# Kernel optimization log

Hardware: AMD Instinct MI355X
Metric: run time of the kernel (lower is better)

The kernel has to match this reference:

```python
import jax, jax.numpy as jnp
import numpy as np

N = 100000   # nodes
E = 800000   # directed edges
IN = 256     # in_channels (== hidden, required by repo's vn MLP dims)
HID = 256    # hidden_channels
OUT = 40     # out_channels (arxiv classes)
EPS = 1e-5


def setup_inputs() -> dict:
    key = jax.random.key(0)
    ks = jax.random.split(key, 8)
    def nrm(k, shape, scale=0.05):
        return jax.random.normal(k, shape, dtype=jnp.float32) * scale
    return {
        "x": nrm(ks[0], (N, IN), 1.0),
        "edge_index": jax.random.randint(ks[1], (2, E), 0, N, dtype=jnp.int32),
        # GCNConv weights (PyG: x @ W, then normalized aggregation, then + bias)
        "W0": nrm(ks[2], (IN, HID)),  "b0": jnp.zeros((HID,), jnp.float32),
        "W1": nrm(ks[3], (HID, HID)), "b1": jnp.zeros((HID,), jnp.float32),
        "W2": nrm(ks[4], (HID, OUT)), "b2": jnp.zeros((OUT,), jnp.float32),
        # BatchNorm1d affine params (batch-stat math, training mode)
        "bn_g0": jnp.ones((HID,), jnp.float32), "bn_b0": jnp.zeros((HID,), jnp.float32),
        "bn_g1": jnp.ones((HID,), jnp.float32), "bn_b1": jnp.zeros((HID,), jnp.float32),
        # virtual node embedding (init to 0 per reset_parameters)
        "vn_emb": jnp.zeros((1, IN), jnp.float32),
        # mlp_vns[0]: Linear(IN,HID) + LayerNorm(HID) + ReLU
        "vn_W0": nrm(ks[5], (IN, HID)),  "vn_b0": jnp.zeros((HID,), jnp.float32),
        "ln_g0": jnp.ones((HID,), jnp.float32), "ln_b0": jnp.zeros((HID,), jnp.float32),
        # mlp_vns[1]: Linear(HID,HID) + LayerNorm(HID) + ReLU
        "vn_W1": nrm(ks[6], (HID, HID)), "vn_b1": jnp.zeros((HID,), jnp.float32),
        "ln_g1": jnp.ones((HID,), jnp.float32), "ln_b1": jnp.zeros((HID,), jnp.float32),
    }


def _forward(x, edge_index, W0, b0, W1, b1, W2, b2, bn_g0, bn_b0, bn_g1, bn_b1,
             vn_emb, vn_W0, vn_b0, ln_g0, ln_b0, vn_W1, vn_b1, ln_g1, ln_b1):
    src, dst = edge_index[0], edge_index[1]
    # GCN symmetric normalization with self-loops: deg = in-degree + 1
    deg = jax.ops.segment_sum(jnp.ones(src.shape, jnp.float32), dst, num_segments=N) + 1.0
    dis = jax.lax.rsqrt(deg)                       # deg^{-1/2}  [N]
    coef = (dis[src] * dis[dst])[:, None]          # edge norm   [E,1]
    self_coef = (dis * dis)[:, None]               # self-loop norm = deg^{-1}  [N,1]

    def gcn(h, W, b):
        h = h @ W                                             # [N, out]
        agg = jax.ops.segment_sum(h[src] * coef, dst, num_segments=N)
        return agg + h * self_coef + b

    def bn(h, g, bv):  # BatchNorm1d, batch statistics over nodes
        mu = h.mean(0)
        var = ((h - mu) ** 2).mean(0)
        return (h - mu) * jax.lax.rsqrt(var + EPS) * g + bv

    def ln(h, g, bv):  # LayerNorm over last dim
        mu = h.mean(-1, keepdims=True)
        var = ((h - mu) ** 2).mean(-1, keepdims=True)
        return (h - mu) * jax.lax.rsqrt(var + EPS) * g + bv

    vx = vn_emb                                   # [1, IN]
    # layer 0
    h = x + vx                                    # virtual-node broadcast
    h = gcn(h, W0, b0)
    h = jax.nn.relu(bn(h, bn_g0, bn_b0))          # dropout = identity (eval)
    pool = jnp.sum(h, axis=0, keepdims=True)      # global_add_pool
    vx = jax.nn.relu(ln((pool + vx) @ vn_W0 + vn_b0, ln_g0, ln_b0))
    # layer 1
    h = h + vx
    h = gcn(h, W1, b1)
    h = jax.nn.relu(bn(h, bn_g1, bn_b1))
    pool = jnp.sum(h, axis=0, keepdims=True)
    vx = jax.nn.relu(ln((pool + vx) @ vn_W1 + vn_b1, ln_g1, ln_b1))
    # layer 2 (output)
    h = h + vx
    h = gcn(h, W2, b2)
    return jax.nn.log_softmax(h, axis=-1)


def reference(x, edge_index, W0, b0, W1, b1, W2, b2, bn_g0, bn_b0, bn_g1, bn_b1,
              vn_emb, vn_W0, vn_b0, ln_g0, ln_b0, vn_W1, vn_b1, ln_g1, ln_b1):
    return _forward(x, edge_index, W0, b0, W1, b1, W2, b2, bn_g0, bn_b0, bn_g1, bn_b1,
                    vn_emb, vn_W0, vn_b0, ln_g0, ln_b0, vn_W1, vn_b1, ln_g1, ln_b1)
```

## Files before the change

### kernel.cpp

```cpp
#include <hip/hip_runtime.h>
#include <hip/hip_bf16.h>
#include <cstdint>

#define N_NODES 100000
#define N_EDGES 800000
#define CH      256
#define COUT    40
#define COUTP   48
#define EPS     1e-5f
#define SCAN_CHUNK 1024
#define NSCAN_BLK  98
#define AGG_NPW 16
#define AGG_BLOCKS 2048
#define AGG_WAVES  (AGG_BLOCKS * 4)
#define GEMMBLK ((N_NODES + 127) / 128)
#define FILLBLK ((N_EDGES + 511) / 512)

typedef unsigned short u16;
typedef unsigned int   u32;
typedef short s16x8 __attribute__((ext_vector_type(8)));
typedef float f32x4 __attribute__((ext_vector_type(4)));

__device__ __forceinline__ float b2f(u32 u) { return __uint_as_float(u << 16); }
__device__ __forceinline__ u16 f2b(float f) {
    u32 u = __float_as_uint(f);
    u32 r = (u + 0x7fffu + ((u >> 16) & 1u)) >> 16;
    return (u16)r;
}
__device__ __forceinline__ u32 packb(float a, float b) {
    return (u32)f2b(a) | ((u32)f2b(b) << 16);
}
__device__ __forceinline__ void unpack8(uint4 v, float* f) {
    f[0] = b2f(v.x & 0xffffu); f[1] = b2f(v.x >> 16);
    f[2] = b2f(v.y & 0xffffu); f[3] = b2f(v.y >> 16);
    f[4] = b2f(v.z & 0xffffu); f[5] = b2f(v.z >> 16);
    f[6] = b2f(v.w & 0xffffu); f[7] = b2f(v.w >> 16);
}

__global__ void k_scan1(const int* __restrict__ counts, int* __restrict__ partial,
                        int* __restrict__ blocksums) {
    __shared__ int sdata[256];
    int base = blockIdx.x * SCAN_CHUNK;
    int t = threadIdx.x;
    int v[4]; int s = 0;
    for (int j = 0; j < 4; j++) {
        int i = base + t * 4 + j;
        v[j] = (i < N_NODES) ? counts[i] : 0;
        s += v[j];
    }
    sdata[t] = s; __syncthreads();
    for (int off = 1; off < 256; off <<= 1) {
        int x = (t >= off) ? sdata[t - off] : 0;
        __syncthreads();
        sdata[t] += x;
        __syncthreads();
    }
    int incl = sdata[t];
    int run = incl - s;
    if (t == 255) blocksums[blockIdx.x] = incl;
    for (int j = 0; j < 4; j++) {
        int i = base + t * 4 + j;
        if (i < N_NODES) partial[i] = run;
        run += v[j];
    }
}

__global__ void k_scan3(int* __restrict__ row_start, const int* __restrict__ blocksums,
                        int* __restrict__ cursor, const int* __restrict__ counts,
                        float* __restrict__ dis) {
    __shared__ int sd[128], raw[128];
    int t = threadIdx.x;
    if (t < 128) {
        int v = (t < NSCAN_BLK) ? blocksums[t] : 0;
        sd[t] = v; raw[t] = v;
    }
    __syncthreads();
    for (int off = 1; off < 128; off <<= 1) {
        int x = (t < 128 && t >= off) ? sd[t - off] : 0;
        __syncthreads();
        if (t < 128) sd[t] += x;
        __syncthreads();
    }
    int i = blockIdx.x * 256 + t;
    if (i < N_NODES) {
        int j = i >> 10;
        int v = row_start[i] + (sd[j] - raw[j]);
        row_start[i] = v;
        cursor[i] = v;
        dis[i] = rsqrtf(1.0f + (float)counts[i]);
    }
}

#define PREP_ZBASE (513 + COUTP)
#define PREP_ZN    (2560 + 2560)
#define PREP_CBASE (PREP_ZBASE + (PREP_ZN + 255) / 256)
#define PREP_CNTBLK ((N_EDGES + 255) / 256)
#define PREP_BLOCKS (PREP_CBASE + PREP_CNTBLK)
__global__ void k_prep(const float* __restrict__ W0, const float* __restrict__ W1,
                       const float* __restrict__ W2,
                       u16* __restrict__ T0, u16* __restrict__ T1, u16* __restrict__ T2,
                       const float* __restrict__ vec, float* __restrict__ v20,
                       int* __restrict__ counts, float* __restrict__ statsA,
                       float* __restrict__ statsB, const int* __restrict__ dst) {
    __shared__ float s[256];
    int b = blockIdx.x, t = threadIdx.x;
    if (b < 256) {
        T0[b * 256 + t] = f2b(W0[t * 256 + b]);
    } else if (b < 512) {
        int n = b - 256;
        T1[n * 256 + t] = f2b(W1[t * 256 + n]);
    } else if (b < 512 + COUTP) {
        int n = b - 512;
        T2[n * 256 + t] = f2b(n < COUT ? W2[t * COUT + n] : 0.f);
    } else if (b == 512 + COUTP) {
        s[t] = vec[t];
        __syncthreads();
        float acc = 0.f;
        for (int k = 0; k < 256; k++) acc += s[k] * W0[k * 256 + t];
        v20[t] = acc;
    } else if (b < PREP_CBASE) {
        int idx = (b - PREP_ZBASE) * 256 + t;
        if (idx < 2560) statsA[idx] = 0.f;
        else if ((idx -= 2560) < 2560) statsB[idx] = 0.f;
    } else {
        int e = (b - PREP_CBASE) * 256 + t;
        if (e < N_EDGES) atomicAdd(&counts[dst[e]], 1);
    }
}

__global__ __launch_bounds__(512) void k_gemm0_fill(const float* __restrict__ A,
                                                    const u16* __restrict__ Wt,
                                                    u16* __restrict__ Hout,
                                                    const int* __restrict__ src,
                                                    const int* __restrict__ dst,
                                                    int* __restrict__ cursor,
                                                    int2* __restrict__ edata,
                                                    const float* __restrict__ dis) {
    __shared__ u16 Bs[256 * 72];
    __shared__ u16 As[128 * 72];
    if (blockIdx.x >= GEMMBLK) {
        int e = (blockIdx.x - GEMMBLK) * 512 + threadIdx.x;
        if (e < N_EDGES) {
            int d = dst[e], s = src[e];
            int p = atomicAdd(&cursor[d], 1);
            int2 v; v.x = s; v.y = __float_as_int(dis[s] * dis[d]);
            edata[p] = v;
        }
        return;
    }
    const int t = threadIdx.x;
    const int wave = t >> 6, lane = t & 63;
    const int lm = lane & 15, quad = lane >> 4;
    const int wr = wave & 1, wc = wave >> 1;
    const int m0 = blockIdx.x * 128;
    const int ar = t >> 2, as_ = (t & 3) * 16;
    const int arow = m0 + ar;
    const int brow = t >> 1, bo = (t & 1) * 32;
    const f32x4 vz = {0.f, 0.f, 0.f, 0.f};
    f32x4 acc[4][4];
    for (int m = 0; m < 4; m++)
        for (int c = 0; c < 4; c++) acc[m][c] = vz;

    for (int k0 = 0; k0 < 256; k0 += 64) {
        {
            const uint4* bsrc = (const uint4*)(Wt + brow * 256 + k0 + bo);
            uint4* bdst = (uint4*)(Bs + brow * 72 + bo);
#pragma unroll
            for (int j = 0; j < 4; j++) bdst[j] = bsrc[j];
            uint4 p0 = {0,0,0,0}, p1 = {0,0,0,0};
            if (arow < N_NODES) {
                const float4* asrc = (const float4*)(A + (size_t)arow * 256 + k0 + as_);
                float4 x0 = asrc[0], x1 = asrc[1], x2 = asrc[2], x3 = asrc[3];
                p0.x = packb(x0.x, x0.y); p0.y = packb(x0.z, x0.w);
                p0.z = packb(x1.x, x1.y); p0.w = packb(x1.z, x1.w);
                p1.x = packb(x2.x, x2.y); p1.y = packb(x2.z, x2.w);
                p1.z = packb(x3.x, x3.y); p1.w = packb(x3.z, x3.w);
            }
            uint4* adst = (uint4*)(As + ar * 72 + as_);
            adst[0] = p0; adst[1] = p1;
        }
        __syncthreads();
#pragma unroll
        for (int kk = 0; kk < 64; kk += 32) {
            s16x8 af[4], bf[4];
#pragma unroll
            for (int m = 0; m < 4; m++)
                af[m] = *(const s16x8*)(As + (wr * 64 + m * 16 + lm) * 72 + kk + quad * 8);
#pragma unroll
            for (int c = 0; c < 4; c++)
                bf[c] = *(const s16x8*)(Bs + (wc * 64 + c * 16 + lm) * 72 + kk + quad * 8);
#pragma unroll
            for (int c = 0; c < 4; c++)
#pragma unroll
                for (int m = 0; m < 4; m++)
                    acc[m][c] = __builtin_amdgcn_mfma_f32_16x16x32_bf16(af[m], bf[c], acc[m][c], 0, 0, 0);
        }
        __syncthreads();
    }
#pragma unroll
    for (int m = 0; m < 4; m++) {
#pragma unroll
        for (int c = 0; c < 4; c++) {
            int col = wc * 64 + c * 16 + lm;
#pragma unroll
            for (int i = 0; i < 4; i++) {
                int row = m0 + wr * 64 + m * 16 + quad * 4 + i;
                if (row < N_NODES) Hout[(size_t)row * 256 + col] = f2b(acc[m][c][i]);
            }
        }
    }
}

__global__ __launch_bounds__(512) void k_gemm_bn(const u16* __restrict__ A,
                                                 const float* __restrict__ stats,
                                                 const float* __restrict__ g,
                                                 const float* __restrict__ bv,
                                                 const u16* __restrict__ Wt,
                                                 u16* __restrict__ Hout,
                                                 float* __restrict__ pool) {
    __shared__ u16 Bs[256 * 72];
    __shared__ u16 As[128 * 72];
    __shared__ float ggs[256], bcs[256], pls[256];
    const int t = threadIdx.x;
    const int wave = t >> 6, lane = t & 63;
    const int lm = lane & 15, quad = lane >> 4;
    const int wr = wave & 1, wc = wave >> 1;
    const int m0 = blockIdx.x * 128;
    const int ar = t >> 2, as_ = (t & 3) * 16;
    const int arow = m0 + ar;
    const int brow = t >> 1, bo = (t & 1) * 32;
    if (t < 256) {
        const float inv = 1.0f / (float)N_NODES;
        float mu = stats[t] * inv;
        float var = stats[256 + t] * inv - mu * mu;
        float rs = rsqrtf(var + EPS);
        float gg = g[t] * rs;
        ggs[t] = gg; bcs[t] = bv[t] - mu * gg;
        pls[t] = 0.f;
    }
    __syncthreads();
    const f32x4 vz = {0.f, 0.f, 0.f, 0.f};
    f32x4 acc[4][4];
    for (int m = 0; m < 4; m++)
        for (int c = 0; c < 4; c++) acc[m][c] = vz;

    for (int k0 = 0; k0 < 256; k0 += 64) {
        float f[16];
        {
            const uint4* bsrc = (const uint4*)(Wt + brow * 256 + k0 + bo);
            uint4* bdst = (uint4*)(Bs + brow * 72 + bo);
#pragma unroll
            for (int j = 0; j < 4; j++) bdst[j] = bsrc[j];
            if (arow < N_NODES) {
                const uint4* asrc = (const uint4*)(A + (size_t)arow * 256 + k0 + as_);
                uint4 r0 = asrc[0], r1 = asrc[1];
                unpack8(r0, f); unpack8(r1, f + 8);
#pragma unroll
                for (int j = 0; j < 16; j++) {
                    int c = k0 + as_ + j;
                    f[j] = fmaxf(f[j] * ggs[c] + bcs[c], 0.f);
                }
            } else {
#pragma unroll
                for (int j = 0; j < 16; j++) f[j] = 0.f;
            }
            uint4 p0, p1;
            p0.x = packb(f[0], f[1]);   p0.y = packb(f[2], f[3]);
            p0.z = packb(f[4], f[5]);   p0.w = packb(f[6], f[7]);
            p1.x = packb(f[8], f[9]);   p1.y = packb(f[10], f[11]);
            p1.z = packb(f[12], f[13]); p1.w = packb(f[14], f[15]);
            uint4* adst = (uint4*)(As + ar * 72 + as_);
            adst[0] = p0; adst[1] = p1;
        }
        __syncthreads();
#pragma unroll
        for (int j = 0; j < 16; j++) {
            float v = f[j];
            v += __shfl_xor(v, 4);  v += __shfl_xor(v, 8);
            v += __shfl_xor(v, 16); v += __shfl_xor(v, 32);
            if (lane < 4) atomicAdd(&pls[k0 + lane * 16 + j], v);
        }
#pragma unroll
        for (int kk = 0; kk < 64; kk += 32) {
            s16x8 af[4], bf[4];
#pragma unroll
            for (int m = 0; m < 4; m++)
                af[m] = *(const s16x8*)(As + (wr * 64 + m * 16 + lm) * 72 + kk + quad * 8);
#pragma unroll
            for (int c = 0; c < 4; c++)
                bf[c] = *(const s16x8*)(Bs + (wc * 64 + c * 16 + lm) * 72 + kk + quad * 8);
#pragma unroll
            for (int c = 0; c < 4; c++)
#pragma unroll
                for (int m = 0; m < 4; m++)
                    acc[m][c] = __builtin_amdgcn_mfma_f32_16x16x32_bf16(af[m], bf[c], acc[m][c], 0, 0, 0);
        }
        __syncthreads();
    }
    if (t < 256) atomicAdd(&pool[(blockIdx.x & 7) * 256 + t], pls[t]);
#pragma unroll
    for (int m = 0; m < 4; m++) {
#pragma unroll
        for (int c = 0; c < 4; c++) {
            int col = wc * 64 + c * 16 + lm;
#pragma unroll
            for (int i = 0; i < 4; i++) {
                int row = m0 + wr * 64 + m * 16 + quad * 4 + i;
                if (row < N_NODES) Hout[(size_t)row * 256 + col] = f2b(acc[m][c][i]);
            }
        }
    }
}

__global__ __launch_bounds__(512) void k_gemm2_bn(const u16* __restrict__ A,
                                                  const float* __restrict__ stats,
                                                  const float* __restrict__ g,
                                                  const float* __restrict__ bv,
                                                  const u16* __restrict__ Wt,
                                                  u16* __restrict__ Hout,
                                                  float* __restrict__ pool) {
    __shared__ u16 Bs[48 * 72];
    __shared__ u16 As[128 * 72];
    __shared__ float ggs[256], bcs[256], pls[256];
    const int t = threadIdx.x;
    const int wave = t >> 6, lane = t & 63;
    const int lm = lane & 15, quad = lane >> 4;
    const int m0 = blockIdx.x * 128;
    const int ar = t >> 2, as_ = (t & 3) * 16;
    const int arow = m0 + ar;
    if (t < 256) {
        const float inv = 1.0f / (float)N_NODES;
        float mu = stats[t] * inv;
        float var = stats[256 + t] * inv - mu * mu;
        float rs = rsqrtf(var + EPS);
        float gg = g[t] * rs;
        ggs[t] = gg; bcs[t] = bv[t] - mu * gg;
        pls[t] = 0.f;
    }
    __syncthreads();
    const f32x4 vz = {0.f, 0.f, 0.f, 0.f};
    f32x4 acc[3]; acc[0] = vz; acc[1] = vz; acc[2] = vz;

    for (int k0 = 0; k0 < 256; k0 += 64) {
        float f[16];
        {
            if (t < 48) {
                const uint4* bsrc = (const uint4*)(Wt + t * 256 + k0);
                uint4* bdst = (uint4*)(Bs + t * 72);
#pragma unroll
                for (int j = 0; j < 8; j++) bdst[j] = bsrc[j];
            }
            if (arow < N_NODES) {
                const uint4* asrc = (const uint4*)(A + (size_t)arow * 256 + k0 + as_);
                uint4 r0 = asrc[0], r1 = asrc[1];
                unpack8(r0, f); unpack8(r1, f + 8);
#pragma unroll
                for (int j = 0; j < 16; j++) {
                    int c = k0 + as_ + j;
                    f[j] = fmaxf(f[j] * ggs[c] + bcs[c], 0.f);
                }
            } else {
#pragma unroll
                for (int j = 0; j < 16; j++) f[j] = 0.f;
            }
            uint4 p0, p1;
            p0.x = packb(f[0], f[1]);   p0.y = packb(f[2], f[3]);
            p0.z = packb(f[4], f[5]);   p0.w = packb(f[6], f[7]);
            p1.x = packb(f[8], f[9]);   p1.y = packb(f[10], f[11]);
            p1.z = packb(f[12], f[13]); p1.w = packb(f[14], f[15]);
            uint4* adst = (uint4*)(As + ar * 72 + as_);
            adst[0] = p0; adst[1] = p1;
        }
        __syncthreads();
#pragma unroll
        for (int j = 0; j < 16; j++) {
            float v = f[j];
            v += __shfl_xor(v, 4);  v += __shfl_xor(v, 8);
            v += __shfl_xor(v, 16); v += __shfl_xor(v, 32);
            if (lane < 4) atomicAdd(&pls[k0 + lane * 16 + j], v);
        }
#pragma unroll
        for (int kk = 0; kk < 64; kk += 32) {
            s16x8 af = *(const s16x8*)(As + (wave * 16 + lm) * 72 + kk + quad * 8);
#pragma unroll
            for (int c = 0; c < 3; c++) {
                s16x8 bf = *(const s16x8*)(Bs + (c * 16 + lm) * 72 + kk + quad * 8);
                acc[c] = __builtin_amdgcn_mfma_f32_16x16x32_bf16(af, bf, acc[c], 0, 0, 0);
            }
        }
        __syncthreads();
    }
    if (t < 256) atomicAdd(&pool[(blockIdx.x & 7) * 256 + t], pls[t]);
#pragma unroll
    for (int c = 0; c < 3; c++) {
        int col = c * 16 + lm;
#pragma unroll
        for (int i = 0; i < 4; i++) {
            int row = m0 + wave * 16 + quad * 4 + i;
            if (row < N_NODES) Hout[(size_t)row * COUTP + col] = f2b(acc[c][i]);
        }
    }
}

__global__ __launch_bounds__(256) void k_agg(const u16* __restrict__ H2,
                                             const int* __restrict__ row_start,
                                             const int* __restrict__ counts,
                                             const int2* __restrict__ edata,
                                             const float* __restrict__ dis,
                                             const float* __restrict__ bias,
                                             const float* __restrict__ v2,
                                             u16* __restrict__ OutB,
                                             float* __restrict__ stats) {
    __shared__ float ls[512];
    const int t = threadIdx.x, wave = t >> 6, lane = t & 63;
    const int half = lane >> 5, hl = lane & 31;
    const int ci = hl * 8;
    const float4 bbA = *(const float4*)(bias + ci);
    const float4 bbB = *(const float4*)(bias + ci + 4);
    const float4 vvA = *(const float4*)(v2 + ci);
    const float4 vvB = *(const float4*)(v2 + ci + 4);
    float s[8], q[8];
#pragma unroll
    for (int j = 0; j < 8; j++) { s[j] = 0.f; q[j] = 0.f; }

    const int gwave = blockIdx.x * 4 + wave;
    const int nid = gwave + lane * AGG_WAVES;
    const bool nv = (lane < AGG_NPW) && (nid < N_NODES);
    const int   my_rs = nv ? row_start[nid] : 0;
    const int   my_ct = nv ? counts[nid] : 0;
    const float my_dn = nv ? dis[nid] : 0.f;

    int beg = __shfl(my_rs, 0), cnt = __shfl(my_ct, 0);
    int2 my_e = {0, 0};
    if (lane < cnt) my_e = edata[beg + lane];

    for (int i = 0; i < AGG_NPW; i++) {
        const int node = gwave + i * AGG_WAVES;
        if (node >= N_NODES) break;
        const int2 cur_e = my_e;
        const int  ccnt = cnt, cbeg = beg;
        const float dn = __shfl(my_dn, i);
        const uint4 rs_ = *(const uint4*)(H2 + (size_t)node * 256 + ci);
        if (i + 1 < AGG_NPW && node + AGG_WAVES < N_NODES) {
            beg = __shfl(my_rs, i + 1);
            cnt = __shfl(my_ct, i + 1);
            int2 tmp = {0, 0};
            if (lane < cnt) tmp = edata[beg + lane];
            my_e = tmp;
        }
        const int cnt64 = ccnt < 64 ? ccnt : 64;
        const int cnt8 = (cnt64 + 7) & ~7;
        float a[8];
#pragma unroll
        for (int j = 0; j < 8; j++) a[j] = 0.f;
        float cs = 0.f;
        for (int e = 0; e < cnt8; e += 8) {
            const int   si0 = __shfl(cur_e.x, e + half);
            const int   si1 = __shfl(cur_e.x, e + 2 + half);
            const int   si2 = __shfl(cur_e.x, e + 4 + half);
            const int   si3 = __shfl(cur_e.x, e + 6 + half);
            const float cf0 = __int_as_float(__shfl(cur_e.y, e + half));
            const float cf1 = __int_as_float(__shfl(cur_e.y, e + 2 + half));
            const float cf2 = __int_as_float(__shfl(cur_e.y, e + 4 + half));
            const float cf3 = __int_as_float(__shfl(cur_e.y, e + 6 + half));
            const uint4 r0 = *(const uint4*)(H2 + (size_t)si0 * 256 + ci);
            const uint4 r1 = *(const uint4*)(H2 + (size_t)si1 * 256 + ci);
            const uint4 r2 = *(const uint4*)(H2 + (size_t)si2 * 256 + ci);
            const uint4 r3 = *(const uint4*)(H2 + (size_t)si3 * 256 + ci);
            cs += cf0 + cf1 + cf2 + cf3;
            a[0] += cf0*b2f(r0.x&0xffffu) + cf1*b2f(r1.x&0xffffu) + cf2*b2f(r2.x&0xffffu) + cf3*b2f(r3.x&0xffffu);
            a[1] += cf0*b2f(r0.x>>16)     + cf1*b2f(r1.x>>16)     + cf2*b2f(r2.x>>16)     + cf3*b2f(r3.x>>16);
            a[2] += cf0*b2f(r0.y&0xffffu) + cf1*b2f(r1.y&0xffffu) + cf2*b2f(r2.y&0xffffu) + cf3*b2f(r3.y&0xffffu);
            a[3] += cf0*b2f(r0.y>>16)     + cf1*b2f(r1.y>>16)     + cf2*b2f(r2.y>>16)     + cf3*b2f(r3.y>>16);
            a[4] += cf0*b2f(r0.z&0xffffu) + cf1*b2f(r1.z&0xffffu) + cf2*b2f(r2.z&0xffffu) + cf3*b2f(r3.z&0xffffu);
            a[5] += cf0*b2f(r0.z>>16)     + cf1*b2f(r1.z>>16)     + cf2*b2f(r2.z>>16)     + cf3*b2f(r3.z>>16);
            a[6] += cf0*b2f(r0.w&0xffffu) + cf1*b2f(r1.w&0xffffu) + cf2*b2f(r2.w&0xffffu) + cf3*b2f(r3.w&0xffffu);
            a[7] += cf0*b2f(r0.w>>16)     + cf1*b2f(r1.w>>16)     + cf2*b2f(r2.w>>16)     + cf3*b2f(r3.w>>16);
        }
        if (ccnt > 64) {
            int e2 = 64;
            for (; e2 + 2 <= ccnt; e2 += 2) {
                const int2 ed_ = edata[cbeg + e2 + half];
                const float cf = __int_as_float(ed_.y);
                const uint4 r = *(const uint4*)(H2 + (size_t)ed_.x * 256 + ci);
                cs += cf;
                a[0] += cf*b2f(r.x&0xffffu); a[1] += cf*b2f(r.x>>16);
                a[2] += cf*b2f(r.y&0xffffu); a[3] += cf*b2f(r.y>>16);
                a[4] += cf*b2f(r.z&0xffffu); a[5] += cf*b2f(r.z>>16);
                a[6] += cf*b2f(r.w&0xffffu); a[7] += cf*b2f(r.w>>16);
            }
            if (e2 < ccnt && half == 0) {
                const int2 ed_ = edata[cbeg + e2];
                const float cf = __int_as_float(ed_.y);
                const uint4 r = *(const uint4*)(H2 + (size_t)ed_.x * 256 + ci);
                cs += cf;
                a[0] += cf*b2f(r.x&0xffffu); a[1] += cf*b2f(r.x>>16);
                a[2] += cf*b2f(r.y&0xffffu); a[3] += cf*b2f(r.y>>16);
                a[4] += cf*b2f(r.z&0xffffu); a[5] += cf*b2f(r.z>>16);
                a[6] += cf*b2f(r.w&0xffffu); a[7] += cf*b2f(r.w>>16);
            }
        }
        cs += __shfl_xor(cs, 32);
#pragma unroll
        for (int j = 0; j < 8; j++) a[j] += __shfl_xor(a[j], 32);
        const float sc = dn * dn, cv = cs + sc;
        const float f0 = a[0] + sc*b2f(rs_.x&0xffffu) + cv*vvA.x + bbA.x;
        const float f1 = a[1] + sc*b2f(rs_.x>>16)     + cv*vvA.y + bbA.y;
        const float f2 = a[2] + sc*b2f(rs_.y&0xffffu) + cv*vvA.z + bbA.z;
        const float f3 = a[3] + sc*b2f(rs_.y>>16)     + cv*vvA.w + bbA.w;
        const float f4 = a[4] + sc*b2f(rs_.z&0xffffu) + cv*vvB.x + bbB.x;
        const float f5 = a[5] + sc*b2f(rs_.z>>16)     + cv*vvB.y + bbB.y;
        const float f6 = a[6] + sc*b2f(rs_.w&0xffffu) + cv*vvB.z + bbB.z;
        const float f7 = a[7] + sc*b2f(rs_.w>>16)     + cv*vvB.w + bbB.w;
        if (half == 0) {
            uint4 o;
            o.x = packb(f0, f1); o.y = packb(f2, f3);
            o.z = packb(f4, f5); o.w = packb(f6, f7);
            *(uint4*)(OutB + (size_t)node * 256 + ci) = o;
        }
        s[0] += f0; q[0] += f0*f0;  s[1] += f1; q[1] += f1*f1;
        s[2] += f2; q[2] += f2*f2;  s[3] += f3; q[3] += f3*f3;
        s[4] += f4; q[4] += f4*f4;  s[5] += f5; q[5] += f5*f5;
        s[6] += f6; q[6] += f6*f6;  s[7] += f7; q[7] += f7*f7;
    }
    ls[t] = 0.f; ls[256 + t] = 0.f;
    __syncthreads();
    if (half == 0) {
#pragma unroll
        for (int j = 0; j < 8; j++) {
            atomicAdd(&ls[ci + j], s[j]);
            atomicAdd(&ls[256 + ci + j], q[j]);
        }
    }
    __syncthreads();
    atomicAdd(&stats[t], ls[t]);
    atomicAdd(&stats[256 + t], ls[256 + t]);
}

__global__ void k_vx(const float* __restrict__ pool, const float* __restrict__ vx_old,
                     const float* __restrict__ vnW, const float* __restrict__ vnb,
                     const float* __restrict__ lng, const float* __restrict__ lnb,
                     float* __restrict__ vx_new,
                     const float* __restrict__ Wnext, int ncn, int npn,
                     float* __restrict__ v2n) {
    __shared__ float s[256];
    __shared__ float red[256];
    int t = threadIdx.x;
    float pv = 0.f;
#pragma unroll
    for (int r = 0; r < 8; r++) pv += pool[r * 256 + t];
    s[t] = pv + vx_old[t];
    __syncthreads();
    float y = vnb[t];
    for (int k = 0; k < 256; k++) y += s[k] * vnW[k * 256 + t];
    red[t] = y; __syncthreads();
    for (int off = 128; off > 0; off >>= 1) {
        if (t < off) red[t] += red[t + off];
        __syncthreads();
    }
    float mu = red[0] * (1.f / 256.f);
    __syncthreads();
    float d = y - mu;
    red[t] = d * d; __syncthreads();
    for (int off = 128; off > 0; off >>= 1) {
        if (t < off) red[t] += red[t + off];
        __syncthreads();
    }
    float var = red[0] * (1.f / 256.f);
    float v = fmaxf(d * rsqrtf(var + EPS) * lng[t] + lnb[t], 0.f);
    vx_new[t] = v;
    __syncthreads();
    s[t] = v;
    __syncthreads();
    float acc = 0.f;
    if (t < ncn) {
        for (int k = 0; k < 256; k++) acc += s[k] * Wnext[k * ncn + t];
    }
    if (t < npn) v2n[t] = acc;
}

__global__ __launch_bounds__(256) void k_agg2(const u16* __restrict__ H2,
                                              const int* __restrict__ row_start,
                                              const int* __restrict__ counts,
                                              const int2* __restrict__ edata,
                                              const float* __restrict__ dis,
                                              const float* __restrict__ bias,
                                              const float* __restrict__ v2,
                                              float* __restrict__ OutF) {
    const int t = threadIdx.x, wave = t >> 6, lane = t & 63;
    const int half = lane >> 5, hl = lane & 31;
    const bool gact = hl < 24;
    const bool cact = hl < 20;
    const int c0 = 2 * hl;
    float bb0 = 0.f, bb1 = 0.f, vv0 = 0.f, vv1 = 0.f;
    if (cact) {
        float2 bv = *(const float2*)(bias + c0); bb0 = bv.x; bb1 = bv.y;
        float2 vvv = *(const float2*)(v2 + c0);  vv0 = vvv.x; vv1 = vvv.y;
    }
    const int nbase = blockIdx.x * 16 + wave * 4;
    for (int i = 0; i < 4; i++) {
        const int node = nbase + i;
        const int beg = row_start[node], cnt = counts[node];
        const float dn = dis[node];
        float a0 = 0.f, a1 = 0.f, cs = 0.f;
        int e = half;
        for (; e + 6 < cnt; e += 8) {
            int2 ea = edata[beg+e],   eb = edata[beg+e+2];
            int2 ec = edata[beg+e+4], ed = edata[beg+e+6];
            float ca = __int_as_float(ea.y), cb = __int_as_float(eb.y);
            float cc = __int_as_float(ec.y), cd = __int_as_float(ed.y);
            u32 ra = 0, rb = 0, rc = 0, rd = 0;
            if (gact) {
                ra = *(const u32*)(H2 + (size_t)ea.x * COUTP + c0);
                rb = *(const u32*)(H2 + (size_t)eb.x * COUTP + c0);
                rc = *(const u32*)(H2 + (size_t)ec.x * COUTP + c0);
                rd = *(const u32*)(H2 + (size_t)ed.x * COUTP + c0);
            }
            cs += ca + cb + cc + cd;
            a0 += ca*b2f(ra&0xffffu) + cb*b2f(rb&0xffffu) + cc*b2f(rc&0xffffu) + cd*b2f(rd&0xffffu);
            a1 += ca*b2f(ra>>16)     + cb*b2f(rb>>16)     + cc*b2f(rc>>16)     + cd*b2f(rd>>16);
        }
        for (; e < cnt; e += 2) {
            int2 ea = edata[beg+e];
            float ca = __int_as_float(ea.y);
            u32 ra = gact ? *(const u32*)(H2 + (size_t)ea.x * COUTP + c0) : 0u;
            cs += ca;
            a0 += ca*b2f(ra&0xffffu); a1 += ca*b2f(ra>>16);
        }
        a0 += __shfl_xor(a0, 32);
        a1 += __shfl_xor(a1, 32);
        cs += __shfl_xor(cs, 32);
        const float sc = dn * dn;
        u32 rs_ = gact ? *(const u32*)(H2 + (size_t)node * COUTP + c0) : 0u;
        float h0 = a0 + sc*b2f(rs_&0xffffu) + (cs+sc)*vv0 + bb0;
        float h1 = a1 + sc*b2f(rs_>>16)     + (cs+sc)*vv1 + bb1;
        float m = cact ? fmaxf(h0, h1) : -3.0e38f;
#pragma unroll
        for (int off = 16; off > 0; off >>= 1) m = fmaxf(m, __shfl_xor(m, off));
        float ex = cact ? (expf(h0 - m) + expf(h1 - m)) : 0.f;
        float se = ex;
#pragma unroll
        for (int off = 16; off > 0; off >>= 1) se += __shfl_xor(se, off);
        float lg = logf(se);
        if (cact && half == 0) {
            float2 o = {h0 - m - lg, h1 - m - lg};
            *(float2*)(OutF + (size_t)node * COUT + c0) = o;
        }
    }
}

extern "C" void kernel_launch(void* const* d_in, const int* in_sizes, int n_in,
                              void* d_out, int out_size, void* d_ws, size_t ws_size,
                              hipStream_t stream) {
    const float* x   = (const float*)d_in[0];
    const int*   ei  = (const int*)d_in[1];
    const int*   esrc = ei;
    const int*   edst = ei + N_EDGES;
    const float* W0 = (const float*)d_in[2];  const float* b0 = (const float*)d_in[3];
    const float* W1 = (const float*)d_in[4];  const float* b1 = (const float*)d_in[5];
    const float* W2 = (const float*)d_in[6];  const float* b2 = (const float*)d_in[7];
    const float* bg0 = (const float*)d_in[8]; const float* bb0 = (const float*)d_in[9];
    const float* bg1 = (const float*)d_in[10]; const float* bb1 = (const float*)d_in[11];
    const float* vn_emb = (const float*)d_in[12];
    const float* vW0 = (const float*)d_in[13]; const float* vb0 = (const float*)d_in[14];
    const float* lg0 = (const float*)d_in[15]; const float* lb0 = (const float*)d_in[16];
    const float* vW1 = (const float*)d_in[17]; const float* vb1 = (const float*)d_in[18];
    const float* lg1 = (const float*)d_in[19]; const float* lb1 = (const float*)d_in[20];

    char* w = (char*)d_ws;
    auto alloc = [&](size_t bytes) { void* p = (void*)w; w += ((bytes + 255) / 256) * 256; return p; };
    u16* H2    = (u16*)alloc((size_t)N_NODES * 256 * 2);
    u16* OutB  = (u16*)alloc((size_t)N_NODES * 256 * 2);
    int2* edata = (int2*)alloc((size_t)N_EDGES * 8);
    int* counts = (int*)alloc((size_t)N_NODES * 4);
    int* rowst  = (int*)alloc((size_t)N_NODES * 4);
    int* cursor = (int*)alloc((size_t)N_NODES * 4);
    float* dis  = (float*)alloc((size_t)N_NODES * 4);
    u16* Wtb0 = (u16*)alloc(256 * 256 * 2);
    u16* Wtb1 = (u16*)alloc(256 * 256 * 2);
    u16* Wt2b = (u16*)alloc(COUTP * 256 * 2);
    int* scanblk = (int*)alloc(128 * 4);
    float* statsA = (float*)alloc(2560 * 4);
    float* statsB = (float*)alloc(2560 * 4);
    float* vxA = (float*)alloc(256 * 4);
    float* vxB = (float*)alloc(256 * 4);
    float* v20 = (float*)alloc(256 * 4);
    float* v21 = (float*)alloc(256 * 4);
    float* v22 = (float*)alloc(64 * 4);
    (void)ws_size; (void)in_sizes; (void)n_in; (void)out_size;

    hipMemsetAsync(counts, 0, (size_t)N_NODES * 4, stream);
    k_prep<<<PREP_BLOCKS, 256, 0, stream>>>(W0, W1, W2, Wtb0, Wtb1, Wt2b,
                                            vn_emb, v20, counts, statsA, statsB, edst);
    k_scan1<<<NSCAN_BLK, 256, 0, stream>>>(counts, rowst, scanblk);
    k_scan3<<<(N_NODES + 255) / 256, 256, 0, stream>>>(rowst, scanblk, cursor, counts, dis);

    k_gemm0_fill<<<GEMMBLK + FILLBLK, 512, 0, stream>>>(x, Wtb0, H2,
                                                        esrc, edst, cursor, edata, dis);
    k_agg<<<AGG_BLOCKS, 256, 0, stream>>>(H2, rowst, counts, edata, dis, b0, v20, OutB, statsA);
    k_gemm_bn<<<GEMMBLK, 512, 0, stream>>>(OutB, statsA, bg0, bb0, Wtb1, H2, statsA + 512);
    k_vx<<<1, 256, 0, stream>>>(statsA + 512, vn_emb, vW0, vb0, lg0, lb0, vxA, W1, 256, 256, v21);
    k_agg<<<AGG_BLOCKS, 256, 0, stream>>>(H2, rowst, counts, edata, dis, b1, v21, OutB, statsB);
    k_gemm2_bn<<<GEMMBLK, 512, 0, stream>>>(OutB, statsB, bg1, bb1, Wt2b, H2, statsB + 512);
    k_vx<<<1, 256, 0, stream>>>(statsB + 512, vxA, vW1, vb1, lg1, lb1, vxB, W2, COUT, COUTP, v22);
    k_agg2<<<N_NODES / 16, 256, 0, stream>>>(H2, rowst, counts, edata, dis, b2, v22, (float*)d_out);
}
```

Measured before the change: 696.6 us.

## Fuse scan into single-pass decoupled kernel and fold vx MLP into GEMM tail

Replaces the two-kernel prefix scan with one kernel in which blocks publish their totals through flagged slots and spin on earlier blocks' totals. It also removes the two single-block k_vx launches by running the virtual-node MLP in whichever GEMM block finishes last, detected with an atomic done-counter. The aim is to cut kernel launches and tail serialization. The cost is spin-waiting, which assumes all 98 scan blocks are resident at once, and a serial tail of work inside the last GEMM block.

```diff
diff --git a/kernel.cpp b/kernel.cpp
--- a/kernel.cpp
+++ b/kernel.cpp
@@ -10,6 +10,7 @@
 #define EPS     1e-5f
 #define SCAN_CHUNK 1024
 #define NSCAN_BLK  98
+#define SCAN_FLAG  0x40000000
 #define AGG_NPW 16
 #define AGG_BLOCKS 2048
 #define AGG_WAVES  (AGG_BLOCKS * 4)
@@ -37,62 +38,8 @@
     f[6] = b2f(v.w & 0xffffu); f[7] = b2f(v.w >> 16);
 }
 
-__global__ void k_scan1(const int* __restrict__ counts, int* __restrict__ partial,
-                        int* __restrict__ blocksums) {
-    __shared__ int sdata[256];
-    int base = blockIdx.x * SCAN_CHUNK;
-    int t = threadIdx.x;
-    int v[4]; int s = 0;
-    for (int j = 0; j < 4; j++) {
-        int i = base + t * 4 + j;
-        v[j] = (i < N_NODES) ? counts[i] : 0;
-        s += v[j];
-    }
-    sdata[t] = s; __syncthreads();
-    for (int off = 1; off < 256; off <<= 1) {
-        int x = (t >= off) ? sdata[t - off] : 0;
-        __syncthreads();
-        sdata[t] += x;
-        __syncthreads();
-    }
-    int incl = sdata[t];
-    int run = incl - s;
-    if (t == 255) blocksums[blockIdx.x] = incl;
-    for (int j = 0; j < 4; j++) {
-        int i = base + t * 4 + j;
-        if (i < N_NODES) partial[i] = run;
-        run += v[j];
-    }
-}
-
-__global__ void k_scan3(int* __restrict__ row_start, const int* __restrict__ blocksums,
-                        int* __restrict__ cursor, const int* __restrict__ counts,
-                        float* __restrict__ dis) {
-    __shared__ int sd[128], raw[128];
-    int t = threadIdx.x;
-    if (t < 128) {
-        int v = (t < NSCAN_BLK) ? blocksums[t] : 0;
-        sd[t] = v; raw[t] = v;
-    }
-    __syncthreads();
-    for (int off = 1; off < 128; off <<= 1) {
-        int x = (t < 128 && t >= off) ? sd[t - off] : 0;
-        __syncthreads();
-        if (t < 128) sd[t] += x;
-        __syncthreads();
-    }
-    int i = blockIdx.x * 256 + t;
-    if (i < N_NODES) {
-        int j = i >> 10;
-        int v = row_start[i] + (sd[j] - raw[j]);
-        row_start[i] = v;
-        cursor[i] = v;
-        dis[i] = rsqrtf(1.0f + (float)counts[i]);
-    }
-}
-
 #define PREP_ZBASE (513 + COUTP)
-#define PREP_ZN    (2560 + 2560)
+#define PREP_ZN    (2564 + 2564 + 128)
 #define PREP_CBASE (PREP_ZBASE + (PREP_ZN + 255) / 256)
 #define PREP_CNTBLK ((N_EDGES + 255) / 256)
 #define PREP_BLOCKS (PREP_CBASE + PREP_CNTBLK)
@@ -101,7 +48,8 @@
                        u16* __restrict__ T0, u16* __restrict__ T1, u16* __restrict__ T2,
                        const float* __restrict__ vec, float* __restrict__ v20,
                        int* __restrict__ counts, float* __restrict__ statsA,
-                       float* __restrict__ statsB, const int* __restrict__ dst) {
+                       float* __restrict__ statsB, int* __restrict__ pub,
+                       const int* __restrict__ dst) {
     __shared__ float s[256];
     int b = blockIdx.x, t = threadIdx.x;
     if (b < 256) {
@@ -120,11 +68,59 @@
         v20[t] = acc;
     } else if (b < PREP_CBASE) {
         int idx = (b - PREP_ZBASE) * 256 + t;
-        if (idx < 2560) statsA[idx] = 0.f;
-        else if ((idx -= 2560) < 2560) statsB[idx] = 0.f;
+        if (idx < 2564) statsA[idx] = 0.f;
+        else if ((idx -= 2564) < 2564) statsB[idx] = 0.f;
+        else if ((idx -= 2564) < 128) pub[idx] = 0;
     } else {
         int e = (b - PREP_CBASE) * 256 + t;
         if (e < N_EDGES) atomicAdd(&counts[dst[e]], 1);
+    }
+}
+
+__global__ void k_scan(const int* __restrict__ counts, int* __restrict__ row_start,
+                       int* __restrict__ cursor, float* __restrict__ dis,
+                       int* __restrict__ pub) {
+    __shared__ int sdata[256];
+    __shared__ int red[256];
+    const int b = blockIdx.x, t = threadIdx.x;
+    const int base = b * SCAN_CHUNK;
+    int v[4]; int s = 0;
+    for (int j = 0; j < 4; j++) {
+        int i = base + t * 4 + j;
+        v[j] = (i < N_NODES) ? counts[i] : 0;
+        s += v[j];
+    }
+    sdata[t] = s; __syncthreads();
+    for (int off = 1; off < 256; off <<= 1) {
+        int x = (t >= off) ? sdata[t - off] : 0;
+        __syncthreads();
+        sdata[t] += x;
+        __syncthreads();
+    }
+    const int incl = sdata[t];
+    const int total = sdata[255];
+    if (t == 0) atomicExch(&pub[b], total | SCAN_FLAG);
+    int part = 0;
+    if (t < b) {
+        volatile int* pp = pub + t;
+        int x_;
+        do { x_ = *pp; } while (!(x_ & SCAN_FLAG));
+        part = x_ & ~SCAN_FLAG;
+    }
+    red[t] = part; __syncthreads();
+    for (int off = 128; off > 0; off >>= 1) {
+        if (t < off) red[t] += red[t + off];
+        __syncthreads();
+    }
+    int run = red[0] + incl - s;
+    for (int j = 0; j < 4; j++) {
+        int i = base + t * 4 + j;
+        if (i < N_NODES) {
+            row_start[i] = run;
+            cursor[i] = run;
+            dis[i] = rsqrtf(1.0f + (float)v[j]);
+        }
+        run += v[j];
     }
 }
 
@@ -217,10 +213,21 @@
                                                  const float* __restrict__ bv,
                                                  const u16* __restrict__ Wt,
                                                  u16* __restrict__ Hout,
-                                                 float* __restrict__ pool) {
+                                                 float* __restrict__ pool,
+                                                 const float* __restrict__ vx_old,
+                                                 const float* __restrict__ vnW,
+                                                 const float* __restrict__ vnb,
+                                                 const float* __restrict__ lng,
+                                                 const float* __restrict__ lnb,
+                                                 float* __restrict__ vx_new,
+                                                 const float* __restrict__ Wnext,
+                                                 int ncn, int npn,
+                                                 float* __restrict__ v2n,
+                                                 int* __restrict__ donectr) {
     __shared__ u16 Bs[256 * 72];
     __shared__ u16 As[128 * 72];
     __shared__ float ggs[256], bcs[256], pls[256];
+    __shared__ int lastf;
     const int t = threadIdx.x;
     const int wave = t >> 6, lane = t & 63;
     const int lm = lane & 15, quad = lane >> 4;
@@ -310,6 +317,52 @@
             }
         }
     }
+    __threadfence();
+    __syncthreads();
+    if (t == 0) lastf = (atomicAdd(donectr, 1) == GEMMBLK - 1) ? 1 : 0;
+    __syncthreads();
+    if (!lastf) return;
+    if (t < 256) {
+        float pv = 0.f;
+#pragma unroll
+        for (int r = 0; r < 8; r++) pv += atomicAdd(&pool[r * 256 + t], 0.f);
+        ggs[t] = pv + vx_old[t];
+    }
+    __syncthreads();
+    float y = 0.f;
+    if (t < 256) {
+        y = vnb[t];
+        for (int k = 0; k < 256; k++) y += ggs[k] * vnW[k * 256 + t];
+        bcs[t] = y;
+    }
+    __syncthreads();
+    for (int off = 128; off > 0; off >>= 1) {
+        if (t < off) bcs[t] += bcs[t + off];
+        __syncthreads();
+    }
+    float mu = bcs[0] * (1.f / 256.f);
+    __syncthreads();
+    float d = y - mu;
+    if (t < 256) bcs[t] = d * d;
+    __syncthreads();
+    for (int off = 128; off > 0; off >>= 1) {
+        if (t < off) bcs[t] += bcs[t + off];
+        __syncthreads();
+    }
+    float var = bcs[0] * (1.f / 256.f);
+    __syncthreads();
+    float vvx = 0.f;
+    if (t < 256) {
+        vvx = fmaxf(d * rsqrtf(var + EPS) * lng[t] + lnb[t], 0.f);
+        vx_new[t] = vvx;
+        ggs[t] = vvx;
+    }
+    __syncthreads();
+    float acc2 = 0.f;
+    if (t < ncn) {
+        for (int k = 0; k < 256; k++) acc2 += ggs[k] * Wnext[k * ncn + t];
+    }
+    if (t < npn) v2n[t] = acc2;
 }
 
 __global__ __launch_bounds__(512) void k_gemm2_bn(const u16* __restrict__ A,
@@ -318,10 +371,21 @@
                                                   const float* __restrict__ bv,
                                                   const u16* __restrict__ Wt,
                                                   u16* __restrict__ Hout,
-                                                  float* __restrict__ pool) {
+                                                  float* __restrict__ pool,
+                                                  const float* __restrict__ vx_old,
+                                                  const float* __restrict__ vnW,
+                                                  const float* __restrict__ vnb,
+                                                  const float* __restrict__ lng,
+                                                  const float* __restrict__ lnb,
+                                                  float* __restrict__ vx_new,
+                                                  const float* __restrict__ Wnext,
+                                                  int ncn, int npn,
+                                                  float* __restrict__ v2n,
+                                                  int* __restrict__ donectr) {
     __shared__ u16 Bs[48 * 72];
     __shared__ u16 As[128 * 72];
     __shared__ float ggs[256], bcs[256], pls[256];
+    __shared__ int lastf;
     const int t = threadIdx.x;
     const int wave = t >> 6, lane = t & 63;
     const int lm = lane & 15, quad = lane >> 4;
@@ -400,6 +464,52 @@
             if (row < N_NODES) Hout[(size_t)row * COUTP + col] = f2b(acc[c][i]);
         }
     }
+    __threadfence();
+    __syncthreads();
+    if (t == 0) lastf = (atomicAdd(donectr, 1) == GEMMBLK - 1) ? 1 : 0;
+    __syncthreads();
+    if (!lastf) return;
+    if (t < 256) {
+        float pv = 0.f;
+#pragma unroll
+        for (int r = 0; r < 8; r++) pv += atomicAdd(&pool[r * 256 + t], 0.f);
+        ggs[t] = pv + vx_old[t];
+    }
+    __syncthreads();
+    float y = 0.f;
+    if (t < 256) {
+        y = vnb[t];
+        for (int k = 0; k < 256; k++) y += ggs[k] * vnW[k * 256 + t];
+        bcs[t] = y;
+    }
+    __syncthreads();
+    for (int off = 128; off > 0; off >>= 1) {
+        if (t < off) bcs[t] += bcs[t + off];
+        __syncthreads();
+    }
+    float mu = bcs[0] * (1.f / 256.f);
+    __syncthreads();
+    float d = y - mu;
+    if (t < 256) bcs[t] = d * d;
+    __syncthreads();
+    for (int off = 128; off > 0; off >>= 1) {
+        if (t < off) bcs[t] += bcs[t + off];
+        __syncthreads();
+    }
+    float var = bcs[0] * (1.f / 256.f);
+    __syncthreads();
+    float vvx = 0.f;
+    if (t < 256) {
+        vvx = fmaxf(d * rsqrtf(var + EPS) * lng[t] + lnb[t], 0.f);
+        vx_new[t] = vvx;
+        ggs[t] = vvx;
+    }
+    __syncthreads();
+    float acc2 = 0.f;
+    if (t < ncn) {
+        for (int k = 0; k < 256; k++) acc2 += ggs[k] * Wnext[k * ncn + t];
+    }
+    if (t < npn) v2n[t] = acc2;
 }
 
 __global__ __launch_bounds__(256) void k_agg(const u16* __restrict__ H2,
@@ -537,48 +647,6 @@
     atomicAdd(&stats[256 + t], ls[256 + t]);
 }
 
-__global__ void k_vx(const float* __restrict__ pool, const float* __restrict__ vx_old,
-                     const float* __restrict__ vnW, const float* __restrict__ vnb,
-                     const float* __restrict__ lng, const float* __restrict__ lnb,
-                     float* __restrict__ vx_new,
-                     const float* __restrict__ Wnext, int ncn, int npn,
-                     float* __restrict__ v2n) {
-    __shared__ float s[256];
-    __shared__ float red[256];
-    int t = threadIdx.x;
-    float pv = 0.f;
-#pragma unroll
-    for (int r = 0; r < 8; r++) pv += pool[r * 256 + t];
-    s[t] = pv + vx_old[t];
-    __syncthreads();
-    float y = vnb[t];
-    for (int k = 0; k < 256; k++) y += s[k] * vnW[k * 256 + t];
-    red[t] = y; __syncthreads();
-    for (int off = 128; off > 0; off >>= 1) {
-        if (t < off) red[t] += red[t + off];
-        __syncthreads();
-    }
-    float mu = red[0] * (1.f / 256.f);
-    __syncthreads();
-    float d = y - mu;
-    red[t] = d * d; __syncthreads();
-    for (int off = 128; off > 0; off >>= 1) {
-        if (t < off) red[t] += red[t + off];
-        __syncthreads();
-    }
-    float var = red[0] * (1.f / 256.f);
-    float v = fmaxf(d * rsqrtf(var + EPS) * lng[t] + lnb[t], 0.f);
-    vx_new[t] = v;
-    __syncthreads();
-    s[t] = v;
-    __syncthreads();
-    float acc = 0.f;
-    if (t < ncn) {
-        for (int k = 0; k < 256; k++) acc += s[k] * Wnext[k * ncn + t];
-    }
-    if (t < npn) v2n[t] = acc;
-}
-
 __global__ __launch_bounds__(256) void k_agg2(const u16* __restrict__ H2,
                                               const int* __restrict__ row_start,
                                               const int* __restrict__ counts,
@@ -680,8 +748,8 @@
     u16* Wtb1 = (u16*)alloc(256 * 256 * 2);
     u16* Wt2b = (u16*)alloc(COUTP * 256 * 2);
     int* scanblk = (int*)alloc(128 * 4);
-    float* statsA = (float*)alloc(2560 * 4);
-    float* statsB = (float*)alloc(2560 * 4);
+    float* statsA = (float*)alloc(2564 * 4);
+    float* statsB = (float*)alloc(2564 * 4);
     float* vxA = (float*)alloc(256 * 4);
     float* vxB = (float*)alloc(256 * 4);
     float* v20 = (float*)alloc(256 * 4);
@@ -691,17 +759,19 @@
 
     hipMemsetAsync(counts, 0, (size_t)N_NODES * 4, stream);
     k_prep<<<PREP_BLOCKS, 256, 0, stream>>>(W0, W1, W2, Wtb0, Wtb1, Wt2b,
-                                            vn_emb, v20, counts, statsA, statsB, edst);
-    k_scan1<<<NSCAN_BLK, 256, 0, stream>>>(counts, rowst, scanblk);
-    k_scan3<<<(N_NODES + 255) / 256, 256, 0, stream>>>(rowst, scanblk, cursor, counts, dis);
+                                            vn_emb, v20, counts, statsA, statsB,
+                                            scanblk, edst);
+    k_scan<<<NSCAN_BLK, 256, 0, stream>>>(counts, rowst, cursor, dis, scanblk);
 
     k_gemm0_fill<<<GEMMBLK + FILLBLK, 512, 0, stream>>>(x, Wtb0, H2,
                                                         esrc, edst, cursor, edata, dis);
     k_agg<<<AGG_BLOCKS, 256, 0, stream>>>(H2, rowst, counts, edata, dis, b0, v20, OutB, statsA);
-    k_gemm_bn<<<GEMMBLK, 512, 0, stream>>>(OutB, statsA, bg0, bb0, Wtb1, H2, statsA + 512);
-    k_vx<<<1, 256, 0, stream>>>(statsA + 512, vn_emb, vW0, vb0, lg0, lb0, vxA, W1, 256, 256, v21);
+    k_gemm_bn<<<GEMMBLK, 512, 0, stream>>>(OutB, statsA, bg0, bb0, Wtb1, H2, statsA + 512,
+                                           vn_emb, vW0, vb0, lg0, lb0, vxA, W1, 256, 256,
+                                           v21, (int*)(statsA + 2560));
     k_agg<<<AGG_BLOCKS, 256, 0, stream>>>(H2, rowst, counts, edata, dis, b1, v21, OutB, statsB);
-    k_gemm2_bn<<<GEMMBLK, 512, 0, stream>>>(OutB, statsB, bg1, bb1, Wt2b, H2, statsB + 512);
-    k_vx<<<1, 256, 0, stream>>>(statsB + 512, vxA, vW1, vb1, lg1, lb1, vxB, W2, COUT, COUTP, v22);
+    k_gemm2_bn<<<GEMMBLK, 512, 0, stream>>>(OutB, statsB, bg1, bb1, Wt2b, H2, statsB + 512,
+                                            vxA, vW1, vb1, lg1, lb1, vxB, W2, COUT, COUTP,
+                                            v22, (int*)(statsB + 2560));
     k_agg2<<<N_NODES / 16, 256, 0, stream>>>(H2, rowst, counts, edata, dis, b2, v22, (float*)d_out);
 }
```

Result: slower. 1.063 ms (+52.6%).
